# Kernel tuning notes

Measured on AMD Instinct MI355X. Metric: run time of the kernel, lower is better.

Reference implementation:

```python
import jax, jax.numpy as jnp
import numpy as np
from jax import lax

B, T, H = 2, 1024, 2048
NH, D = 8, 128          # heads, head_dim
P = NH * D              # projection size
K = 4                   # short conv kernel size
EPS = 1e-6
SCALE = D ** -0.5


def _causal_conv_silu(x, w):
    # x: (B,T,C); w: (C,K) depthwise causal conv followed by silu (ShortConvolution)
    C = w.shape[0]
    kern = jnp.transpose(w)[:, None, :]  # (K,1,C)
    y = lax.conv_general_dilated(x, kern, window_strides=(1,), padding=[(K - 1, 0)],
                                 dimension_numbers=('NWC', 'WIO', 'NWC'),
                                 feature_group_count=C)
    return jax.nn.silu(y)


def _l2norm(x):
    return x * jax.lax.rsqrt(jnp.sum(x * x, axis=-1, keepdims=True) + EPS)


def _forward(hidden_states, Wq, Wk, Wv, conv_q, conv_k, conv_v, A_log, dt_bias,
             Wfa, Wfb, Wb, Wga, Wgb, norm_weight, Wo):
    x = hidden_states                                # (B,T,H)
    q = _causal_conv_silu(x @ Wq.T, conv_q)          # (B,T,P)
    k = _causal_conv_silu(x @ Wk.T, conv_k)
    v = _causal_conv_silu(x @ Wv.T, conv_v)
    # fused_kda_gate: g = -exp(A_log) * softplus(f_b(f_a(x)) + dt_bias), per (h,d) channel
    gf = (x @ Wfa.T) @ Wfb.T                         # (B,T,P) low-rank gate proj
    gf = gf.reshape(B, T, NH, D) + dt_bias.reshape(NH, D)
    g = -jnp.exp(A_log)[None, None, :, None] * jax.nn.softplus(gf)  # (B,T,NH,D) log-decay <= 0
    beta = jax.nn.sigmoid(x @ Wb.T)                  # (B,T,NH)
    q = _l2norm(q.reshape(B, T, NH, D)) * SCALE      # use_qk_l2norm_in_kernel + 1/sqrt(d) scale
    k = _l2norm(k.reshape(B, T, NH, D))
    v = v.reshape(B, T, NH, D)

    # gated delta-rule recurrence (KDA): per-key-channel decay, beta-weighted delta update
    def step(S, inp):
        q_t, k_t, v_t, g_t, b_t = inp                # (B,NH,D), beta (B,NH)
        S = S * jnp.exp(g_t)[..., None]              # decay rows (key dim) of S[.,.,dk,dv]
        kv = jnp.einsum('bhk,bhkv->bhv', k_t, S)
        delta = (v_t - kv) * b_t[..., None]
        S = S + jnp.einsum('bhk,bhv->bhkv', k_t, delta)
        o_t = jnp.einsum('bhk,bhkv->bhv', q_t, S)
        return S, o_t

    tfirst = lambda a: jnp.moveaxis(a, 1, 0)         # time-major for scan
    S0 = jnp.zeros((B, NH, D, D), x.dtype)
    _, o = lax.scan(step, S0, (tfirst(q), tfirst(k), tfirst(v), tfirst(g), tfirst(beta)))
    o = jnp.moveaxis(o, 0, 1)                        # (B,T,NH,D)

    # FusedRMSNormGated(sigmoid): gate applied before RMS normalization (Mamba2 convention)
    gate = ((x @ Wga.T) @ Wgb.T).reshape(B, T, NH, D)
    og = o * jax.nn.sigmoid(gate)
    og = og * jax.lax.rsqrt(jnp.mean(og * og, axis=-1, keepdims=True) + EPS) * norm_weight
    return og.reshape(B * T, P) @ Wo.T               # (B*T, H)


def setup_inputs():
    ks = jax.random.split(jax.random.key(0), 16)
    s = 0.02
    f32 = jnp.float32
    return {
        'hidden_states': jax.random.normal(ks[0], (B, T, H), f32),
        'Wq': jax.random.normal(ks[1], (P, H), f32) * s,
        'Wk': jax.random.normal(ks[2], (P, H), f32) * s,
        'Wv': jax.random.normal(ks[3], (P, H), f32) * s,
        'conv_q': jax.random.normal(ks[4], (P, K), f32) * 0.3,
        'conv_k': jax.random.normal(ks[5], (P, K), f32) * 0.3,
        'conv_v': jax.random.normal(ks[6], (P, K), f32) * 0.3,
        'A_log': jnp.log(jax.random.uniform(ks[7], (NH,), f32, 1.0, 16.0)),
        'dt_bias': jax.random.normal(ks[8], (P,), f32) * 0.5,
        'Wfa': jax.random.normal(ks[9], (D, H), f32) * s,
        'Wfb': jax.random.normal(ks[10], (P, D), f32) * s,
        'Wb': jax.random.normal(ks[11], (NH, H), f32) * s,
        'Wga': jax.random.normal(ks[12], (D, H), f32) * s,
        'Wgb': jax.random.normal(ks[13], (P, D), f32) * s,
        'norm_weight': jnp.ones((D,), f32),
        'Wo': jax.random.normal(ks[14], (H, P), f32) * s,
    }


def reference(hidden_states, Wq, Wk, Wv, conv_q, conv_k, conv_v, A_log, dt_bias,
              Wfa, Wfb, Wb, Wga, Wgb, norm_weight, Wo):
    return _forward(hidden_states, Wq, Wk, Wv, conv_q, conv_k, conv_v, A_log, dt_bias,
                    Wfa, Wfb, Wb, Wga, Wgb, norm_weight, Wo)
```

## Files before the change

### kernel.cpp

```cpp
#include <hip/hip_runtime.h>
#include <hip/hip_bf16.h>
#include <cstddef>
#include <cstdint>

#define Bb 2
#define Tt 1024
#define Hh 2048
#define NHh 8
#define Dd 128
#define Pp (NHh * Dd)
#define Kk 4
#define EPSf 1e-6f
#define SCALEf 0.08838834764831845f
#define DVQ 16
#define CHUNK 8

typedef short bf16x8 __attribute__((ext_vector_type(8)));
typedef float f32x4 __attribute__((ext_vector_type(4)));

template <int CTRL>
__device__ __forceinline__ float dpp_add(float x) {
  int yi = __builtin_amdgcn_update_dpp(0, __builtin_bit_cast(int, x), CTRL, 0xF, 0xF, true);
  return x + __builtin_bit_cast(float, yi);
}
__device__ __forceinline__ float row16_sum(float x) {
  x = dpp_add<0xB1>(x);
  x = dpp_add<0x4E>(x);
  x = dpp_add<0x124>(x);
  x = dpp_add<0x128>(x);
  return x;
}

__device__ __forceinline__ void gload_lds16(const void* g, void* l) {
  __builtin_amdgcn_global_load_lds((const __attribute__((address_space(1))) void*)g,
                                   (__attribute__((address_space(3))) void*)l, 16, 0, 0);
}

__global__ __launch_bounds__(256) void cvt_bf16(const float* __restrict__ src,
                                                __hip_bfloat16* __restrict__ dst, int n) {
  const int i = (blockIdx.x * 256 + threadIdx.x) * 8;
  if (i >= n) return;
  const float4 a = *reinterpret_cast<const float4*>(src + i);
  const float4 b = *reinterpret_cast<const float4*>(src + i + 4);
  __hip_bfloat16 t[8];
  t[0] = __float2bfloat16(a.x); t[1] = __float2bfloat16(a.y);
  t[2] = __float2bfloat16(a.z); t[3] = __float2bfloat16(a.w);
  t[4] = __float2bfloat16(b.x); t[5] = __float2bfloat16(b.y);
  t[6] = __float2bfloat16(b.z); t[7] = __float2bfloat16(b.w);
  *reinterpret_cast<uint4*>(dst + i) = *reinterpret_cast<const uint4*>(t);
}

__global__ __launch_bounds__(256) void cvt_split(const float* __restrict__ src,
                                                 __hip_bfloat16* __restrict__ hi,
                                                 __hip_bfloat16* __restrict__ lo, int n) {
  const int i = (blockIdx.x * 256 + threadIdx.x) * 8;
  if (i >= n) return;
  __hip_bfloat16 th[8], tl[8];
#pragma unroll
  for (int j = 0; j < 2; j++) {
    const float4 a = *reinterpret_cast<const float4*>(src + i + j * 4);
    const float f[4] = {a.x, a.y, a.z, a.w};
#pragma unroll
    for (int e = 0; e < 4; e++) {
      const __hip_bfloat16 h = __float2bfloat16(f[e]);
      th[j * 4 + e] = h;
      tl[j * 4 + e] = __float2bfloat16(f[e] - __bfloat162float(h));
    }
  }
  *reinterpret_cast<uint4*>(hi + i) = *reinterpret_cast<const uint4*>(th);
  *reinterpret_cast<uint4*>(lo + i) = *reinterpret_cast<const uint4*>(tl);
}

__global__ __launch_bounds__(256) void transpose_f32(const float* __restrict__ src,
                                                     float* __restrict__ dst, int R, int C) {
  __shared__ float t[32][33];
  const int bx = blockIdx.x * 32, by = blockIdx.y * 32;
  const int tx = threadIdx.x & 31, ty = threadIdx.x >> 5;
#pragma unroll
  for (int i = ty; i < 32; i += 8) {
    const int r = by + i, c = bx + tx;
    if (r < R && c < C) t[i][tx] = src[(size_t)r * C + c];
  }
  __syncthreads();
#pragma unroll
  for (int i = ty; i < 32; i += 8) {
    const int c = bx + i, r = by + tx;
    if (c < C && r < R) dst[(size_t)c * R + r] = t[tx][i];
  }
}

__global__ __launch_bounds__(256) void gemm_bf16_lds(const __hip_bfloat16* __restrict__ A,
                                                     const __hip_bfloat16* __restrict__ B,
                                                     float* __restrict__ C,
                                                     __hip_bfloat16* __restrict__ Cbf,
                                                     int M, int N, int K, int outmode) {
  __shared__ __align__(16) __hip_bfloat16 As[128 * 64];
  __shared__ __align__(16) __hip_bfloat16 Bs[128 * 64];
  const int tid = threadIdx.x;
  const int wave = tid >> 6;
  const int lane = tid & 63;
  const int wm = (wave >> 1) * 64;
  const int wn = (wave & 1) * 64;
  const int bm = blockIdx.y * 128;
  const int bn = blockIdx.x * 128;
  const int l15 = lane & 15;
  const int l4 = lane >> 4;
  const int srow = lane >> 3;
  const int scol = (lane & 7) * 8;

  f32x4 acc[4][4];
#pragma unroll
  for (int i = 0; i < 4; i++)
#pragma unroll
    for (int j = 0; j < 4; j++) acc[i][j] = (f32x4){0.f, 0.f, 0.f, 0.f};

  for (int k0 = 0; k0 < K; k0 += 64) {
#pragma unroll
    for (int i = 0; i < 4; i++) {
      const int s = wave * 4 + i;
      const int row = s * 8 + srow;
      gload_lds16(A + (size_t)(bm + row) * K + k0 + scol, &As[s * 512]);
      gload_lds16(B + (size_t)(bn + row) * K + k0 + scol, &Bs[s * 512]);
    }
    __syncthreads();
    bf16x8 af[4][2], bfv[4][2];
#pragma unroll
    for (int kf = 0; kf < 2; kf++) {
      const int kc = kf * 32 + l4 * 8;
#pragma unroll
      for (int mf = 0; mf < 4; mf++)
        af[mf][kf] = *reinterpret_cast<const bf16x8*>(&As[(wm + mf * 16 + l15) * 64 + kc]);
#pragma unroll
      for (int nf = 0; nf < 4; nf++)
        bfv[nf][kf] = *reinterpret_cast<const bf16x8*>(&Bs[(wn + nf * 16 + l15) * 64 + kc]);
    }
#pragma unroll
    for (int kf = 0; kf < 2; kf++)
#pragma unroll
      for (int mf = 0; mf < 4; mf++)
#pragma unroll
        for (int nf = 0; nf < 4; nf++)
          acc[mf][nf] = __builtin_amdgcn_mfma_f32_16x16x32_bf16(af[mf][kf], bfv[nf][kf],
                                                                acc[mf][nf], 0, 0, 0);
    __syncthreads();
  }
#pragma unroll
  for (int mf = 0; mf < 4; mf++) {
#pragma unroll
    for (int nf = 0; nf < 4; nf++) {
      const int col = bn + wn + nf * 16 + l15;
#pragma unroll
      for (int r = 0; r < 4; r++) {
        const int row = bm + wm + mf * 16 + l4 * 4 + r;
        if (outmode == 0) C[(size_t)row * N + col] = acc[mf][nf][r];
        else Cbf[(size_t)row * N + col] = __float2bfloat16(acc[mf][nf][r]);
      }
    }
  }
}

#define LDT3 40
__global__ __launch_bounds__(256) void gemm_bf16_3t(const __hip_bfloat16* __restrict__ Ahi,
                                                    const __hip_bfloat16* __restrict__ Alo,
                                                    const __hip_bfloat16* __restrict__ Bhi,
                                                    const __hip_bfloat16* __restrict__ Blo,
                                                    float* __restrict__ C,
                                                    int M, int N, int K) {
  __shared__ __align__(16) __hip_bfloat16 Ahs[64][LDT3];
  __shared__ __align__(16) __hip_bfloat16 Als[64][LDT3];
  __shared__ __align__(16) __hip_bfloat16 Bhs[128][LDT3];
  __shared__ __align__(16) __hip_bfloat16 Bls[128][LDT3];
  const int tid = threadIdx.x;
  const int wave = tid >> 6;
  const int lane = tid & 63;
  const int wm = (wave >> 1) * 32;
  const int wn = (wave & 1) * 64;
  const int bm = blockIdx.y * 64;
  const int bn = blockIdx.x * 128;
  const int l15 = lane & 15;
  const int l4 = lane >> 4;
  const int arow = tid >> 2;
  const int acol = (tid & 3) * 8;

  f32x4 acc[2][4];
#pragma unroll
  for (int i = 0; i < 2; i++)
#pragma unroll
    for (int j = 0; j < 4; j++) acc[i][j] = (f32x4){0.f, 0.f, 0.f, 0.f};

  for (int k0 = 0; k0 < K; k0 += 32) {
    uint4 rah, ral, rbh0, rbh1, rbl0, rbl1;
    rah  = *reinterpret_cast<const uint4*>(Ahi + (size_t)(bm + arow) * K + k0 + acol);
    ral  = *reinterpret_cast<const uint4*>(Alo + (size_t)(bm + arow) * K + k0 + acol);
    rbh0 = *reinterpret_cast<const uint4*>(Bhi + (size_t)(bn + arow) * K + k0 + acol);
    rbh1 = *reinterpret_cast<const uint4*>(Bhi + (size_t)(bn + arow + 64) * K + k0 + acol);
    rbl0 = *reinterpret_cast<const uint4*>(Blo + (size_t)(bn + arow) * K + k0 + acol);
    rbl1 = *reinterpret_cast<const uint4*>(Blo + (size_t)(bn + arow + 64) * K + k0 + acol);
    __syncthreads();
    *reinterpret_cast<uint4*>(&Ahs[arow][acol]) = rah;
    *reinterpret_cast<uint4*>(&Als[arow][acol]) = ral;
    *reinterpret_cast<uint4*>(&Bhs[arow][acol]) = rbh0;
    *reinterpret_cast<uint4*>(&Bhs[arow + 64][acol]) = rbh1;
    *reinterpret_cast<uint4*>(&Bls[arow][acol]) = rbl0;
    *reinterpret_cast<uint4*>(&Bls[arow + 64][acol]) = rbl1;
    __syncthreads();
    const int kc = l4 * 8;
    bf16x8 ah[2], al[2], bhf[4], blf[4];
#pragma unroll
    for (int mf = 0; mf < 2; mf++) {
      ah[mf] = *reinterpret_cast<const bf16x8*>(&Ahs[wm + mf * 16 + l15][kc]);
      al[mf] = *reinterpret_cast<const bf16x8*>(&Als[wm + mf * 16 + l15][kc]);
    }
#pragma unroll
    for (int nf = 0; nf < 4; nf++) {
      bhf[nf] = *reinterpret_cast<const bf16x8*>(&Bhs[wn + nf * 16 + l15][kc]);
      blf[nf] = *reinterpret_cast<const bf16x8*>(&Bls[wn + nf * 16 + l15][kc]);
    }
#pragma unroll
    for (int mf = 0; mf < 2; mf++)
#pragma unroll
      for (int nf = 0; nf < 4; nf++) {
        acc[mf][nf] = __builtin_amdgcn_mfma_f32_16x16x32_bf16(ah[mf], bhf[nf], acc[mf][nf], 0, 0, 0);
        acc[mf][nf] = __builtin_amdgcn_mfma_f32_16x16x32_bf16(ah[mf], blf[nf], acc[mf][nf], 0, 0, 0);
        acc[mf][nf] = __builtin_amdgcn_mfma_f32_16x16x32_bf16(al[mf], bhf[nf], acc[mf][nf], 0, 0, 0);
      }
  }
#pragma unroll
  for (int mf = 0; mf < 2; mf++)
#pragma unroll
    for (int nf = 0; nf < 4; nf++) {
      const int col = bn + wn + nf * 16 + l15;
#pragma unroll
      for (int r = 0; r < 4; r++) {
        const int row = bm + wm + mf * 16 + l4 * 4 + r;
        C[(size_t)row * N + col] = acc[mf][nf][r];
      }
    }
}

__global__ __launch_bounds__(256) void gemm_nt(const float* __restrict__ A,
                                               const float* __restrict__ Bm,
                                               float* __restrict__ C,
                                               int M, int N, int Kd) {
  __shared__ float As[16][64];
  __shared__ float Bs[16][64];
  const int bm = blockIdx.y * 64;
  const int bn = blockIdx.x * 64;
  const int tid = threadIdx.x;
  const int tx = tid & 15;
  const int ty = tid >> 4;
  const int lr = tid >> 2;
  const int lc = (tid & 3) << 2;
  float acc[4][4];
#pragma unroll
  for (int i = 0; i < 4; i++)
#pragma unroll
    for (int j = 0; j < 4; j++) acc[i][j] = 0.f;
  for (int k0 = 0; k0 < Kd; k0 += 16) {
    float4 a4 = make_float4(0.f, 0.f, 0.f, 0.f);
    float4 b4 = make_float4(0.f, 0.f, 0.f, 0.f);
    const int ar = bm + lr;
    if (ar < M) a4 = *reinterpret_cast<const float4*>(A + (size_t)ar * Kd + k0 + lc);
    const int br = bn + lr;
    if (br < N) b4 = *reinterpret_cast<const float4*>(Bm + (size_t)br * Kd + k0 + lc);
    As[lc + 0][lr] = a4.x; As[lc + 1][lr] = a4.y; As[lc + 2][lr] = a4.z; As[lc + 3][lr] = a4.w;
    Bs[lc + 0][lr] = b4.x; Bs[lc + 1][lr] = b4.y; Bs[lc + 2][lr] = b4.z; Bs[lc + 3][lr] = b4.w;
    __syncthreads();
#pragma unroll
    for (int kk = 0; kk < 16; kk++) {
      float4 av = *reinterpret_cast<const float4*>(&As[kk][ty << 2]);
      float4 bv = *reinterpret_cast<const float4*>(&Bs[kk][tx << 2]);
      float a[4] = {av.x, av.y, av.z, av.w};
      float b[4] = {bv.x, bv.y, bv.z, bv.w};
#pragma unroll
      for (int i = 0; i < 4; i++)
#pragma unroll
        for (int j = 0; j < 4; j++) acc[i][j] += a[i] * b[j];
    }
    __syncthreads();
  }
#pragma unroll
  for (int i = 0; i < 4; i++) {
    const int row = bm + (ty << 2) + i;
    if (row >= M) continue;
#pragma unroll
    for (int j = 0; j < 4; j++) {
      const int col = bn + (tx << 2) + j;
      if (col < N) C[(size_t)row * N + col] = acc[i][j];
    }
  }
}

__global__ __launch_bounds__(256) void beta_kernel(const float* __restrict__ x,
                                                   const float* __restrict__ Wb,
                                                   float* __restrict__ beta) {
  __shared__ float xs[Hh];
  const int m = blockIdx.x;
  const int tid = threadIdx.x;
  for (int i = tid; i < Hh; i += 256) xs[i] = x[(size_t)m * Hh + i];
  __syncthreads();
  const int h = tid >> 5;
  const int lane = tid & 31;
  float acc = 0.f;
  for (int i = lane; i < Hh; i += 32) acc += xs[i] * Wb[(size_t)h * Hh + i];
#pragma unroll
  for (int o = 16; o > 0; o >>= 1) acc += __shfl_down(acc, o, 32);
  if (lane == 0) beta[(size_t)m * NHh + h] = 1.f / (1.f + expf(-acc));
}

__global__ __launch_bounds__(256) void g_kernel(float* __restrict__ gbuf,
                                                const float* __restrict__ dtb,
                                                const float* __restrict__ A_log) {
  const size_t i = (size_t)blockIdx.x * 256 + threadIdx.x;
  const int c = (int)(i % Pp);
  const int h = c / Dd;
  const float xv = gbuf[i] + dtb[c];
  const float sp = (xv > 20.f) ? xv : log1pf(expf(xv));
  gbuf[i] = expf(-expf(A_log[h]) * sp);
}

__global__ __launch_bounds__(128) void conv_silu_norm(const float* __restrict__ xin,
                                                      const float* __restrict__ w,
                                                      float* __restrict__ out,
                                                      int mode, int instride, int coff) {
  const int idx = blockIdx.x;
  const int h = idx % NHh;
  const int bt = idx / NHh;
  const int t = bt % Tt;
  const int d = threadIdx.x;
  const int c = h * Dd + d;
  float acc = 0.f;
#pragma unroll
  for (int j = 0; j < Kk; j++) {
    const int tt = t - (Kk - 1) + j;
    float xv = 0.f;
    if (tt >= 0) xv = xin[(size_t)(bt - (Kk - 1) + j) * instride + coff + c];
    acc += w[c * Kk + j] * xv;
  }
  float y = acc / (1.f + expf(-acc));
  float r = y;
  if (mode > 0) {
    float ss = y * y;
#pragma unroll
    for (int o = 32; o > 0; o >>= 1) ss += __shfl_down(ss, o);
    __shared__ float red[2];
    if ((d & 63) == 0) red[d >> 6] = ss;
    __syncthreads();
    const float tot = red[0] + red[1];
    const float inv = rsqrtf(tot + EPSf);
    r = y * inv * (mode == 2 ? SCALEf : 1.f);
  }
  out[(size_t)bt * Pp + c] = r;
}

__global__ __launch_bounds__(128) void scan_kernel(const float* __restrict__ q,
                                                   const float* __restrict__ k,
                                                   const float* __restrict__ v,
                                                   const float* __restrict__ eg,
                                                   const float* __restrict__ beta,
                                                   float* __restrict__ o) {
  const int blk = blockIdx.x;
  const int bh = blk & 15;
  const int dvq = blk >> 4;
  const int b = bh >> 3, h = bh & 7;
  const int tid = threadIdx.x;
  const int qr = tid & 15;
  const int dvl = tid >> 4;
  const int dv = dvq * 8 + dvl;

  __shared__ __align__(16) float qs[CHUNK][16][12];
  __shared__ __align__(16) float ks[CHUNK][16][12];
  __shared__ __align__(16) float legs[CHUNK][16][12];
  __shared__ float vs[CHUNK][8];
  __shared__ float betas[CHUNK];

  float s[8];
#pragma unroll
  for (int i = 0; i < 8; i++) s[i] = 0.f;

  const size_t base = (size_t)(b * Tt) * Pp + h * Dd;
  const int le = tid;

  float rq[CHUNK], rk[CHUNK], re[CHUNK], rv[CHUNK], rb;
  auto load_chunk = [&](int t0) {
    const size_t coff = base + (size_t)t0 * Pp;
#pragma unroll
    for (int j = 0; j < CHUNK; j++) {
      rq[j] = q[coff + (size_t)j * Pp + le];
      rk[j] = k[coff + (size_t)j * Pp + le];
      re[j] = eg[coff + (size_t)j * Pp + le];
    }
    if (tid < 8) {
#pragma unroll
      for (int j = 0; j < CHUNK; j++) rv[j] = v[coff + (size_t)j * Pp + dvq * 8 + tid];
    } else if (tid < 8 + CHUNK) {
      rb = beta[(size_t)(b * Tt + t0 + tid - 8) * NHh + h];
    }
  };

  load_chunk(0);
  size_t off = base;
  for (int c = 0; c < Tt / CHUNK; c++) {
    __syncthreads();
#pragma unroll
    for (int j = 0; j < CHUNK; j++) {
      qs[j][le >> 3][le & 7] = rq[j];
      ks[j][le >> 3][le & 7] = rk[j];
      legs[j][le >> 3][le & 7] = re[j];
    }
    if (tid < 8) {
#pragma unroll
      for (int j = 0; j < CHUNK; j++) vs[j][tid] = rv[j];
    } else if (tid < 8 + CHUNK) {
      betas[tid - 8] = rb;
    }
    __syncthreads();
    if (c + 1 < Tt / CHUNK) load_chunk((c + 1) * CHUNK);

    float vv[CHUNK], bb[CHUNK], opart[CHUNK];
#pragma unroll
    for (int j = 0; j < CHUNK; j++) { vv[j] = vs[j][dvl]; bb[j] = betas[j]; }

#pragma unroll
    for (int j = 0; j < CHUNK; j++) {
      const float4 k0 = *reinterpret_cast<const float4*>(&ks[j][qr][0]);
      const float4 k1 = *reinterpret_cast<const float4*>(&ks[j][qr][4]);
      const float4 e0 = *reinterpret_cast<const float4*>(&legs[j][qr][0]);
      const float4 e1 = *reinterpret_cast<const float4*>(&legs[j][qr][4]);
      s[0] *= e0.x; s[1] *= e0.y; s[2] *= e0.z; s[3] *= e0.w;
      s[4] *= e1.x; s[5] *= e1.y; s[6] *= e1.z; s[7] *= e1.w;
      float kva = k0.x * s[0] + k1.x * s[4];
      float kvb = k0.y * s[1] + k1.y * s[5];
      float kvc = k0.z * s[2] + k1.z * s[6];
      float kvd = k0.w * s[3] + k1.w * s[7];
      const float kvp = row16_sum((kva + kvb) + (kvc + kvd));
      const float delta = (vv[j] - kvp) * bb[j];
      const float4 q0 = *reinterpret_cast<const float4*>(&qs[j][qr][0]);
      const float4 q1 = *reinterpret_cast<const float4*>(&qs[j][qr][4]);
      s[0] += k0.x * delta; float oa = q0.x * s[0];
      s[1] += k0.y * delta; float ob = q0.y * s[1];
      s[2] += k0.z * delta; float oc = q0.z * s[2];
      s[3] += k0.w * delta; float od = q0.w * s[3];
      s[4] += k1.x * delta; oa += q1.x * s[4];
      s[5] += k1.y * delta; ob += q1.y * s[5];
      s[6] += k1.z * delta; oc += q1.z * s[6];
      s[7] += k1.w * delta; od += q1.w * s[7];
      opart[j] = (oa + ob) + (oc + od);
    }
#pragma unroll
    for (int j = 0; j < CHUNK; j++) opart[j] = row16_sum(opart[j]);
    if (qr == 0) {
#pragma unroll
      for (int j = 0; j < CHUNK; j++) o[off + (size_t)j * Pp + dv] = opart[j];
    }
    off += (size_t)CHUNK * Pp;
  }
}

__global__ __launch_bounds__(128) void gated_norm(float* __restrict__ o,
                                                  const float* __restrict__ gate,
                                                  int gstride,
                                                  const float* __restrict__ nw,
                                                  __hip_bfloat16* __restrict__ ogbf) {
  const int idx = blockIdx.x;
  const int h = idx % NHh;
  const int bt = idx / NHh;
  const int d = threadIdx.x;
  const size_t off = (size_t)bt * Pp + h * Dd;
  const float ov = o[off + d];
  const float gt = gate[(size_t)bt * gstride + h * Dd + d];
  const float val = ov / (1.f + expf(-gt));
  float ss = val * val;
#pragma unroll
  for (int sh = 32; sh > 0; sh >>= 1) ss += __shfl_down(ss, sh);
  __shared__ float red[2];
  if ((d & 63) == 0) red[d >> 6] = ss;
  __syncthreads();
  const float mean = (red[0] + red[1]) * (1.f / Dd);
  const float res = val * rsqrtf(mean + EPSf) * nw[d];
  if (ogbf != nullptr) ogbf[off + d] = __float2bfloat16(res);
  else o[off + d] = res;
}

extern "C" void kernel_launch(void* const* d_in, const int* in_sizes, int n_in,
                              void* d_out, int out_size, void* d_ws, size_t ws_size,
                              hipStream_t stream) {
  const float* x     = (const float*)d_in[0];
  const float* Wq    = (const float*)d_in[1];
  const float* Wk    = (const float*)d_in[2];
  const float* Wv    = (const float*)d_in[3];
  const float* cq    = (const float*)d_in[4];
  const float* ck    = (const float*)d_in[5];
  const float* cv    = (const float*)d_in[6];
  const float* A_log = (const float*)d_in[7];
  const float* dtb   = (const float*)d_in[8];
  const float* Wfa   = (const float*)d_in[9];
  const float* Wfb   = (const float*)d_in[10];
  const float* Wb    = (const float*)d_in[11];
  const float* Wga   = (const float*)d_in[12];
  const float* Wgb   = (const float*)d_in[13];
  const float* nw    = (const float*)d_in[14];
  const float* Wo    = (const float*)d_in[15];
  float* outp = (float*)d_out;

  const int M = Bb * Tt;
  const size_t MP = (size_t)M * Pp;
  float* ws = (float*)d_ws;
  float* qkvpre = ws;
  float* qb   = qkvpre + 4 * MP;
  float* kb   = qb + MP;
  float* vb   = kb + MP;
  float* gbuf = vb + MP;
  float* obuf = gbuf + MP;
  float* betab = obuf + MP;
  float* WfaT = betab + (size_t)M * NHh;
  float* WgaT = WfaT + (size_t)Hh * Dd;
  float* f32end = WgaT + (size_t)Hh * Dd;
  float* Wcombf = obuf;

  __hip_bfloat16* xhi    = (__hip_bfloat16*)f32end;
  __hip_bfloat16* xlo    = xhi + (size_t)M * Hh;
  __hip_bfloat16* Wqkvbf = xlo + (size_t)M * Hh;
  __hip_bfloat16* Wobf   = Wqkvbf + (size_t)4 * Pp * Hh;
  __hip_bfloat16* WfaThi = Wobf + (size_t)Hh * Pp;
  __hip_bfloat16* WfaTlo = WfaThi + (size_t)Hh * Dd;
  __hip_bfloat16* Wfbhi  = WfaTlo + (size_t)Hh * Dd;
  __hip_bfloat16* Wfblo  = Wfbhi + (size_t)Pp * Dd;
  __hip_bfloat16* WgaTbf = Wfblo + (size_t)Pp * Dd;
  __hip_bfloat16* Wgbbf  = WgaTbf + (size_t)Hh * Dd;
  __hip_bfloat16* Wcombhi = Wgbbf + (size_t)Pp * Dd;
  __hip_bfloat16* Wcomblo = Wcombhi + (size_t)Pp * Hh;
  __hip_bfloat16* end = Wcomblo + (size_t)Pp * Hh;
  __hip_bfloat16* ogbf = xlo;
  const bool use_mfma = ws_size >= (size_t)((char*)end - (char*)d_ws);

  const dim3 blk(256);
  if (use_mfma) {
    cvt_split<<<(int)((size_t)M * Hh / 2048), blk, 0, stream>>>(x, xhi, xlo, M * Hh);
    cvt_bf16<<<(int)((size_t)Pp * Hh / 2048), blk, 0, stream>>>(Wq, Wqkvbf, Pp * Hh);
    cvt_bf16<<<(int)((size_t)Pp * Hh / 2048), blk, 0, stream>>>(Wk, Wqkvbf + (size_t)Pp * Hh, Pp * Hh);
    cvt_bf16<<<(int)((size_t)Pp * Hh / 2048), blk, 0, stream>>>(Wv, Wqkvbf + (size_t)2 * Pp * Hh, Pp * Hh);
    cvt_bf16<<<(int)((size_t)Hh * Pp / 2048), blk, 0, stream>>>(Wo, Wobf, Hh * Pp);
    transpose_f32<<<dim3(Hh / 32, Dd / 32), blk, 0, stream>>>(Wfa, WfaT, Dd, Hh);
    transpose_f32<<<dim3(Hh / 32, Dd / 32), blk, 0, stream>>>(Wga, WgaT, Dd, Hh);
    cvt_split<<<(int)((size_t)Hh * Dd / 2048), blk, 0, stream>>>(WfaT, WfaThi, WfaTlo, Hh * Dd);
    cvt_split<<<(int)((size_t)Pp * Dd / 2048), blk, 0, stream>>>(Wfb, Wfbhi, Wfblo, Pp * Dd);
    cvt_bf16<<<(int)((size_t)Hh * Dd / 2048), blk, 0, stream>>>(WgaT, WgaTbf, Hh * Dd);
    cvt_bf16<<<(int)((size_t)Pp * Dd / 2048), blk, 0, stream>>>(Wgb, Wgbbf, Pp * Dd);
    gemm_bf16_3t<<<dim3(Hh / 128, Pp / 64), blk, 0, stream>>>(Wfbhi, Wfblo, WfaThi, WfaTlo,
                                                              Wcombf, Pp, Hh, Dd);
    gemm_bf16_lds<<<dim3(Hh / 128, Pp / 128), blk, 0, stream>>>(Wgbbf, WgaTbf, nullptr,
                                                                Wqkvbf + (size_t)3 * Pp * Hh,
                                                                Pp, Hh, Dd, 1);
    cvt_split<<<(int)((size_t)Pp * Hh / 2048), blk, 0, stream>>>(Wcombf, Wcombhi, Wcomblo, Pp * Hh);
    gemm_bf16_lds<<<dim3(4 * Pp / 128, M / 128), blk, 0, stream>>>(xhi, Wqkvbf, qkvpre, nullptr,
                                                                   M, 4 * Pp, Hh, 0);
    gemm_bf16_3t<<<dim3(Pp / 128, M / 64), blk, 0, stream>>>(xhi, xlo, Wcombhi, Wcomblo,
                                                             gbuf, M, Pp, Hh);
    beta_kernel<<<M, 256, 0, stream>>>(x, Wb, betab);
    g_kernel<<<(int)(MP / 256), 256, 0, stream>>>(gbuf, dtb, A_log);
    conv_silu_norm<<<M * NHh, 128, 0, stream>>>(qkvpre, cq, qb, 2, 4 * Pp, 0);
    conv_silu_norm<<<M * NHh, 128, 0, stream>>>(qkvpre, ck, kb, 1, 4 * Pp, Pp);
    conv_silu_norm<<<M * NHh, 128, 0, stream>>>(qkvpre, cv, vb, 0, 4 * Pp, 2 * Pp);
    scan_kernel<<<Bb * NHh * DVQ, 128, 0, stream>>>(qb, kb, vb, gbuf, betab, obuf);
    gated_norm<<<M * NHh, 128, 0, stream>>>(obuf, qkvpre + (size_t)3 * Pp, 4 * Pp, nw, ogbf);
    gemm_bf16_lds<<<dim3(Hh / 128, M / 128), blk, 0, stream>>>(ogbf, Wobf, outp, nullptr, M, Hh, Pp, 0);
  } else {
    float* qpre = qkvpre;
    float* kpre = qkvpre + MP;
    float* vpre = qkvpre + 2 * MP;
    float* gate = qkvpre + 3 * MP;
    float* gfa = WfaT;
    float* gga = WgaT;
    gemm_nt<<<dim3(Pp / 64, M / 64), blk, 0, stream>>>(x, Wq, qpre, M, Pp, Hh);
    gemm_nt<<<dim3(Pp / 64, M / 64), blk, 0, stream>>>(x, Wk, kpre, M, Pp, Hh);
    gemm_nt<<<dim3(Pp / 64, M / 64), blk, 0, stream>>>(x, Wv, vpre, M, Pp, Hh);
    gemm_nt<<<dim3(Dd / 64, M / 64), blk, 0, stream>>>(x, Wfa, gfa, M, Dd, Hh);
    gemm_nt<<<dim3(Dd / 64, M / 64), blk, 0, stream>>>(x, Wga, gga, M, Dd, Hh);
    gemm_nt<<<dim3(Pp / 64, M / 64), blk, 0, stream>>>(gfa, Wfb, gbuf, M, Pp, Dd);
    gemm_nt<<<dim3(Pp / 64, M / 64), blk, 0, stream>>>(gga, Wgb, gate, M, Pp, Dd);
    beta_kernel<<<M, 256, 0, stream>>>(x, Wb, betab);
    g_kernel<<<(int)(MP / 256), 256, 0, stream>>>(gbuf, dtb, A_log);
    conv_silu_norm<<<M * NHh, 128, 0, stream>>>(qpre, cq, qb, 2, Pp, 0);
    conv_silu_norm<<<M * NHh, 128, 0, stream>>>(kpre, ck, kb, 1, Pp, 0);
    conv_silu_norm<<<M * NHh, 128, 0, stream>>>(vpre, cv, vb, 0, Pp, 0);
    scan_kernel<<<Bb * NHh * DVQ, 128, 0, stream>>>(qb, kb, vb, gbuf, betab, obuf);
    gated_norm<<<M * NHh, 128, 0, stream>>>(obuf, gate, Pp, nw, nullptr);
    gemm_nt<<<dim3(Hh / 64, M / 64), blk, 0, stream>>>(obuf, Wo, outp, M, Hh, Pp);
  }
}
```

Baseline: 486.1 us.

## Double-buffer scan LDS, use direct-to-LDS loads in 3-term GEMM, batch weight casts

```diff
diff --git a/kernel.cpp b/kernel.cpp
--- a/kernel.cpp
+++ b/kernel.cpp
@@ -47,6 +47,30 @@
   t[2] = __float2bfloat16(a.z); t[3] = __float2bfloat16(a.w);
   t[4] = __float2bfloat16(b.x); t[5] = __float2bfloat16(b.y);
   t[6] = __float2bfloat16(b.z); t[7] = __float2bfloat16(b.w);
+  *reinterpret_cast<uint4*>(dst + i) = *reinterpret_cast<const uint4*>(t);
+}
+
+__global__ __launch_bounds__(256) void cvt_bf16_x4(const float* __restrict__ s0,
+                                                   const float* __restrict__ s1,
+                                                   const float* __restrict__ s2,
+                                                   const float* __restrict__ s3,
+                                                   __hip_bfloat16* __restrict__ d0,
+                                                   __hip_bfloat16* __restrict__ d1,
+                                                   __hip_bfloat16* __restrict__ d2,
+                                                   __hip_bfloat16* __restrict__ d3,
+                                                   int nper) {
+  const int bpa = nper / 2048;
+  const int a = blockIdx.x / bpa;
+  const int i = (blockIdx.x % bpa) * 2048 + threadIdx.x * 8;
+  const float* src = (a == 0) ? s0 : (a == 1) ? s1 : (a == 2) ? s2 : s3;
+  __hip_bfloat16* dst = (a == 0) ? d0 : (a == 1) ? d1 : (a == 2) ? d2 : d3;
+  const float4 x = *reinterpret_cast<const float4*>(src + i);
+  const float4 y = *reinterpret_cast<const float4*>(src + i + 4);
+  __hip_bfloat16 t[8];
+  t[0] = __float2bfloat16(x.x); t[1] = __float2bfloat16(x.y);
+  t[2] = __float2bfloat16(x.z); t[3] = __float2bfloat16(x.w);
+  t[4] = __float2bfloat16(y.x); t[5] = __float2bfloat16(y.y);
+  t[6] = __float2bfloat16(y.z); t[7] = __float2bfloat16(y.w);
   *reinterpret_cast<uint4*>(dst + i) = *reinterpret_cast<const uint4*>(t);
 }
 
@@ -159,17 +183,16 @@
   }
 }
 
-#define LDT3 40
-__global__ __launch_bounds__(256) void gemm_bf16_3t(const __hip_bfloat16* __restrict__ Ahi,
-                                                    const __hip_bfloat16* __restrict__ Alo,
-                                                    const __hip_bfloat16* __restrict__ Bhi,
-                                                    const __hip_bfloat16* __restrict__ Blo,
-                                                    float* __restrict__ C,
-                                                    int M, int N, int K) {
-  __shared__ __align__(16) __hip_bfloat16 Ahs[64][LDT3];
-  __shared__ __align__(16) __hip_bfloat16 Als[64][LDT3];
-  __shared__ __align__(16) __hip_bfloat16 Bhs[128][LDT3];
-  __shared__ __align__(16) __hip_bfloat16 Bls[128][LDT3];
+__global__ __launch_bounds__(256) void gemm_bf16_3t_lds(const __hip_bfloat16* __restrict__ Ahi,
+                                                        const __hip_bfloat16* __restrict__ Alo,
+                                                        const __hip_bfloat16* __restrict__ Bhi,
+                                                        const __hip_bfloat16* __restrict__ Blo,
+                                                        float* __restrict__ C,
+                                                        int M, int N, int K) {
+  __shared__ __align__(16) __hip_bfloat16 Ahs[64 * 64];
+  __shared__ __align__(16) __hip_bfloat16 Als[64 * 64];
+  __shared__ __align__(16) __hip_bfloat16 Bhs[128 * 64];
+  __shared__ __align__(16) __hip_bfloat16 Bls[128 * 64];
   const int tid = threadIdx.x;
   const int wave = tid >> 6;
   const int lane = tid & 63;
@@ -179,8 +202,8 @@
   const int bn = blockIdx.x * 128;
   const int l15 = lane & 15;
   const int l4 = lane >> 4;
-  const int arow = tid >> 2;
-  const int acol = (tid & 3) * 8;
+  const int srow = lane >> 3;
+  const int scol = (lane & 7) * 8;
 
   f32x4 acc[2][4];
 #pragma unroll
@@ -188,42 +211,49 @@
 #pragma unroll
     for (int j = 0; j < 4; j++) acc[i][j] = (f32x4){0.f, 0.f, 0.f, 0.f};
 
-  for (int k0 = 0; k0 < K; k0 += 32) {
-    uint4 rah, ral, rbh0, rbh1, rbl0, rbl1;
-    rah  = *reinterpret_cast<const uint4*>(Ahi + (size_t)(bm + arow) * K + k0 + acol);
-    ral  = *reinterpret_cast<const uint4*>(Alo + (size_t)(bm + arow) * K + k0 + acol);
-    rbh0 = *reinterpret_cast<const uint4*>(Bhi + (size_t)(bn + arow) * K + k0 + acol);
-    rbh1 = *reinterpret_cast<const uint4*>(Bhi + (size_t)(bn + arow + 64) * K + k0 + acol);
-    rbl0 = *reinterpret_cast<const uint4*>(Blo + (size_t)(bn + arow) * K + k0 + acol);
-    rbl1 = *reinterpret_cast<const uint4*>(Blo + (size_t)(bn + arow + 64) * K + k0 + acol);
-    __syncthreads();
-    *reinterpret_cast<uint4*>(&Ahs[arow][acol]) = rah;
-    *reinterpret_cast<uint4*>(&Als[arow][acol]) = ral;
-    *reinterpret_cast<uint4*>(&Bhs[arow][acol]) = rbh0;
-    *reinterpret_cast<uint4*>(&Bhs[arow + 64][acol]) = rbh1;
-    *reinterpret_cast<uint4*>(&Bls[arow][acol]) = rbl0;
-    *reinterpret_cast<uint4*>(&Bls[arow + 64][acol]) = rbl1;
-    __syncthreads();
-    const int kc = l4 * 8;
-    bf16x8 ah[2], al[2], bhf[4], blf[4];
-#pragma unroll
-    for (int mf = 0; mf < 2; mf++) {
-      ah[mf] = *reinterpret_cast<const bf16x8*>(&Ahs[wm + mf * 16 + l15][kc]);
-      al[mf] = *reinterpret_cast<const bf16x8*>(&Als[wm + mf * 16 + l15][kc]);
-    }
-#pragma unroll
-    for (int nf = 0; nf < 4; nf++) {
-      bhf[nf] = *reinterpret_cast<const bf16x8*>(&Bhs[wn + nf * 16 + l15][kc]);
-      blf[nf] = *reinterpret_cast<const bf16x8*>(&Bls[wn + nf * 16 + l15][kc]);
-    }
-#pragma unroll
-    for (int mf = 0; mf < 2; mf++)
+  for (int k0 = 0; k0 < K; k0 += 64) {
+#pragma unroll
+    for (int i = 0; i < 12; i++) {
+      const int sid = wave * 12 + i;
+      if (sid < 8) {
+        const int row = sid * 8 + srow;
+        gload_lds16(Ahi + (size_t)(bm + row) * K + k0 + scol, &Ahs[sid * 512]);
+      } else if (sid < 16) {
+        const int row = (sid - 8) * 8 + srow;
+        gload_lds16(Alo + (size_t)(bm + row) * K + k0 + scol, &Als[(sid - 8) * 512]);
+      } else if (sid < 32) {
+        const int row = (sid - 16) * 8 + srow;
+        gload_lds16(Bhi + (size_t)(bn + row) * K + k0 + scol, &Bhs[(sid - 16) * 512]);
+      } else {
+        const int row = (sid - 32) * 8 + srow;
+        gload_lds16(Blo + (size_t)(bn + row) * K + k0 + scol, &Bls[(sid - 32) * 512]);
+      }
+    }
+    __syncthreads();
+#pragma unroll
+    for (int kf = 0; kf < 2; kf++) {
+      const int kc = kf * 32 + l4 * 8;
+      bf16x8 ah[2], al[2], bh[4], bl[4];
+#pragma unroll
+      for (int mf = 0; mf < 2; mf++) {
+        ah[mf] = *reinterpret_cast<const bf16x8*>(&Ahs[(wm + mf * 16 + l15) * 64 + kc]);
+        al[mf] = *reinterpret_cast<const bf16x8*>(&Als[(wm + mf * 16 + l15) * 64 + kc]);
+      }
 #pragma unroll
       for (int nf = 0; nf < 4; nf++) {
-        acc[mf][nf] = __builtin_amdgcn_mfma_f32_16x16x32_bf16(ah[mf], bhf[nf], acc[mf][nf], 0, 0, 0);
-        acc[mf][nf] = __builtin_amdgcn_mfma_f32_16x16x32_bf16(ah[mf], blf[nf], acc[mf][nf], 0, 0, 0);
-        acc[mf][nf] = __builtin_amdgcn_mfma_f32_16x16x32_bf16(al[mf], bhf[nf], acc[mf][nf], 0, 0, 0);
+        bh[nf] = *reinterpret_cast<const bf16x8*>(&Bhs[(wn + nf * 16 + l15) * 64 + kc]);
+        bl[nf] = *reinterpret_cast<const bf16x8*>(&Bls[(wn + nf * 16 + l15) * 64 + kc]);
       }
+#pragma unroll
+      for (int mf = 0; mf < 2; mf++)
+#pragma unroll
+        for (int nf = 0; nf < 4; nf++) {
+          acc[mf][nf] = __builtin_amdgcn_mfma_f32_16x16x32_bf16(ah[mf], bh[nf], acc[mf][nf], 0, 0, 0);
+          acc[mf][nf] = __builtin_amdgcn_mfma_f32_16x16x32_bf16(ah[mf], bl[nf], acc[mf][nf], 0, 0, 0);
+          acc[mf][nf] = __builtin_amdgcn_mfma_f32_16x16x32_bf16(al[mf], bh[nf], acc[mf][nf], 0, 0, 0);
+        }
+    }
+    __syncthreads();
   }
 #pragma unroll
   for (int mf = 0; mf < 2; mf++)
@@ -368,11 +398,11 @@
   const int dvl = tid >> 4;
   const int dv = dvq * 8 + dvl;
 
-  __shared__ __align__(16) float qs[CHUNK][16][12];
-  __shared__ __align__(16) float ks[CHUNK][16][12];
-  __shared__ __align__(16) float legs[CHUNK][16][12];
-  __shared__ float vs[CHUNK][8];
-  __shared__ float betas[CHUNK];
+  __shared__ __align__(16) float qs[2][CHUNK][16][12];
+  __shared__ __align__(16) float ks[2][CHUNK][16][12];
+  __shared__ __align__(16) float legs[2][CHUNK][16][12];
+  __shared__ float vs[2][CHUNK][8];
+  __shared__ float betas[2][CHUNK];
 
   float s[8];
 #pragma unroll
@@ -381,7 +411,7 @@
   const size_t base = (size_t)(b * Tt) * Pp + h * Dd;
   const int le = tid;
 
-  float rq[CHUNK], rk[CHUNK], re[CHUNK], rv[CHUNK], rb;
+  float rq[CHUNK], rk[CHUNK], re[CHUNK], rv[CHUNK], rb = 0.f;
   auto load_chunk = [&](int t0) {
     const size_t coff = base + (size_t)t0 * Pp;
 #pragma unroll
@@ -397,55 +427,75 @@
       rb = beta[(size_t)(b * Tt + t0 + tid - 8) * NHh + h];
     }
   };
+  auto write_lds = [&](int bufw) {
+#pragma unroll
+    for (int j = 0; j < CHUNK; j++) {
+      qs[bufw][j][le >> 3][le & 7] = rq[j];
+      ks[bufw][j][le >> 3][le & 7] = rk[j];
+      legs[bufw][j][le >> 3][le & 7] = re[j];
+    }
+    if (tid < 8) {
+#pragma unroll
+      for (int j = 0; j < CHUNK; j++) vs[bufw][j][tid] = rv[j];
+    } else if (tid < 8 + CHUNK) {
+      betas[bufw][tid - 8] = rb;
+    }
+  };
 
   load_chunk(0);
+  write_lds(0);
+  __syncthreads();
+  const int NC = Tt / CHUNK;
   size_t off = base;
-  for (int c = 0; c < Tt / CHUNK; c++) {
-    __syncthreads();
+  for (int c = 0; c < NC; c++) {
+    if (c + 1 < NC) load_chunk((c + 1) * CHUNK);
+    const int buf = c & 1;
+    float vv[CHUNK], bb[CHUNK], opart[CHUNK];
+#pragma unroll
+    for (int j = 0; j < CHUNK; j++) { vv[j] = vs[buf][j][dvl]; bb[j] = betas[buf][j]; }
+
+    float4 ck0 = *reinterpret_cast<const float4*>(&ks[buf][0][qr][0]);
+    float4 ck1 = *reinterpret_cast<const float4*>(&ks[buf][0][qr][4]);
+    float4 ce0 = *reinterpret_cast<const float4*>(&legs[buf][0][qr][0]);
+    float4 ce1 = *reinterpret_cast<const float4*>(&legs[buf][0][qr][4]);
+    float4 cq0 = *reinterpret_cast<const float4*>(&qs[buf][0][qr][0]);
+    float4 cq1 = *reinterpret_cast<const float4*>(&qs[buf][0][qr][4]);
+    float kt0 = ck0.x * ce0.x, kt1 = ck0.y * ce0.y, kt2 = ck0.z * ce0.z, kt3 = ck0.w * ce0.w;
+    float kt4 = ck1.x * ce1.x, kt5 = ck1.y * ce1.y, kt6 = ck1.z * ce1.z, kt7 = ck1.w * ce1.w;
+
 #pragma unroll
     for (int j = 0; j < CHUNK; j++) {
-      qs[j][le >> 3][le & 7] = rq[j];
-      ks[j][le >> 3][le & 7] = rk[j];
-      legs[j][le >> 3][le & 7] = re[j];
-    }
-    if (tid < 8) {
-#pragma unroll
-      for (int j = 0; j < CHUNK; j++) vs[j][tid] = rv[j];
-    } else if (tid < 8 + CHUNK) {
-      betas[tid - 8] = rb;
-    }
-    __syncthreads();
-    if (c + 1 < Tt / CHUNK) load_chunk((c + 1) * CHUNK);
-
-    float vv[CHUNK], bb[CHUNK], opart[CHUNK];
-#pragma unroll
-    for (int j = 0; j < CHUNK; j++) { vv[j] = vs[j][dvl]; bb[j] = betas[j]; }
-
-#pragma unroll
-    for (int j = 0; j < CHUNK; j++) {
-      const float4 k0 = *reinterpret_cast<const float4*>(&ks[j][qr][0]);
-      const float4 k1 = *reinterpret_cast<const float4*>(&ks[j][qr][4]);
-      const float4 e0 = *reinterpret_cast<const float4*>(&legs[j][qr][0]);
-      const float4 e1 = *reinterpret_cast<const float4*>(&legs[j][qr][4]);
-      s[0] *= e0.x; s[1] *= e0.y; s[2] *= e0.z; s[3] *= e0.w;
-      s[4] *= e1.x; s[5] *= e1.y; s[6] *= e1.z; s[7] *= e1.w;
-      float kva = k0.x * s[0] + k1.x * s[4];
-      float kvb = k0.y * s[1] + k1.y * s[5];
-      float kvc = k0.z * s[2] + k1.z * s[6];
-      float kvd = k0.w * s[3] + k1.w * s[7];
+      float4 nk0, nk1, ne0, ne1, nq0, nq1;
+      if (j + 1 < CHUNK) {
+        nk0 = *reinterpret_cast<const float4*>(&ks[buf][j + 1][qr][0]);
+        nk1 = *reinterpret_cast<const float4*>(&ks[buf][j + 1][qr][4]);
+        ne0 = *reinterpret_cast<const float4*>(&legs[buf][j + 1][qr][0]);
+        ne1 = *reinterpret_cast<const float4*>(&legs[buf][j + 1][qr][4]);
+        nq0 = *reinterpret_cast<const float4*>(&qs[buf][j + 1][qr][0]);
+        nq1 = *reinterpret_cast<const float4*>(&qs[buf][j + 1][qr][4]);
+      }
+      const float es0 = ce0.x * s[0], es1 = ce0.y * s[1], es2 = ce0.z * s[2], es3 = ce0.w * s[3];
+      const float es4 = ce1.x * s[4], es5 = ce1.y * s[5], es6 = ce1.z * s[6], es7 = ce1.w * s[7];
+      float kva = kt0 * s[0] + kt4 * s[4];
+      float kvb = kt1 * s[1] + kt5 * s[5];
+      float kvc = kt2 * s[2] + kt6 * s[6];
+      float kvd = kt3 * s[3] + kt7 * s[7];
       const float kvp = row16_sum((kva + kvb) + (kvc + kvd));
       const float delta = (vv[j] - kvp) * bb[j];
-      const float4 q0 = *reinterpret_cast<const float4*>(&qs[j][qr][0]);
-      const float4 q1 = *reinterpret_cast<const float4*>(&qs[j][qr][4]);
-      s[0] += k0.x * delta; float oa = q0.x * s[0];
-      s[1] += k0.y * delta; float ob = q0.y * s[1];
-      s[2] += k0.z * delta; float oc = q0.z * s[2];
-      s[3] += k0.w * delta; float od = q0.w * s[3];
-      s[4] += k1.x * delta; oa += q1.x * s[4];
-      s[5] += k1.y * delta; ob += q1.y * s[5];
-      s[6] += k1.z * delta; oc += q1.z * s[6];
-      s[7] += k1.w * delta; od += q1.w * s[7];
+      s[0] = fmaf(ck0.x, delta, es0); float oa = cq0.x * s[0];
+      s[1] = fmaf(ck0.y, delta, es1); float ob = cq0.y * s[1];
+      s[2] = fmaf(ck0.z, delta, es2); float oc = cq0.z * s[2];
+      s[3] = fmaf(ck0.w, delta, es3); float od = cq0.w * s[3];
+      s[4] = fmaf(ck1.x, delta, es4); oa += cq1.x * s[4];
+      s[5] = fmaf(ck1.y, delta, es5); ob += cq1.y * s[5];
+      s[6] = fmaf(ck1.z, delta, es6); oc += cq1.z * s[6];
+      s[7] = fmaf(ck1.w, delta, es7); od += cq1.w * s[7];
       opart[j] = (oa + ob) + (oc + od);
+      if (j + 1 < CHUNK) {
+        ck0 = nk0; ck1 = nk1; ce0 = ne0; ce1 = ne1; cq0 = nq0; cq1 = nq1;
+        kt0 = ck0.x * ce0.x; kt1 = ck0.y * ce0.y; kt2 = ck0.z * ce0.z; kt3 = ck0.w * ce0.w;
+        kt4 = ck1.x * ce1.x; kt5 = ck1.y * ce1.y; kt6 = ck1.z * ce1.z; kt7 = ck1.w * ce1.w;
+      }
     }
 #pragma unroll
     for (int j = 0; j < CHUNK; j++) opart[j] = row16_sum(opart[j]);
@@ -453,6 +503,8 @@
 #pragma unroll
       for (int j = 0; j < CHUNK; j++) o[off + (size_t)j * Pp + dv] = opart[j];
     }
+    if (c + 1 < NC) write_lds(buf ^ 1);
+    __syncthreads();
     off += (size_t)CHUNK * Pp;
   }
 }
@@ -537,26 +589,25 @@
   const dim3 blk(256);
   if (use_mfma) {
     cvt_split<<<(int)((size_t)M * Hh / 2048), blk, 0, stream>>>(x, xhi, xlo, M * Hh);
-    cvt_bf16<<<(int)((size_t)Pp * Hh / 2048), blk, 0, stream>>>(Wq, Wqkvbf, Pp * Hh);
-    cvt_bf16<<<(int)((size_t)Pp * Hh / 2048), blk, 0, stream>>>(Wk, Wqkvbf + (size_t)Pp * Hh, Pp * Hh);
-    cvt_bf16<<<(int)((size_t)Pp * Hh / 2048), blk, 0, stream>>>(Wv, Wqkvbf + (size_t)2 * Pp * Hh, Pp * Hh);
-    cvt_bf16<<<(int)((size_t)Hh * Pp / 2048), blk, 0, stream>>>(Wo, Wobf, Hh * Pp);
+    cvt_bf16_x4<<<4 * (int)((size_t)Pp * Hh / 2048), blk, 0, stream>>>(
+        Wq, Wk, Wv, Wo, Wqkvbf, Wqkvbf + (size_t)Pp * Hh, Wqkvbf + (size_t)2 * Pp * Hh,
+        Wobf, Pp * Hh);
     transpose_f32<<<dim3(Hh / 32, Dd / 32), blk, 0, stream>>>(Wfa, WfaT, Dd, Hh);
     transpose_f32<<<dim3(Hh / 32, Dd / 32), blk, 0, stream>>>(Wga, WgaT, Dd, Hh);
     cvt_split<<<(int)((size_t)Hh * Dd / 2048), blk, 0, stream>>>(WfaT, WfaThi, WfaTlo, Hh * Dd);
     cvt_split<<<(int)((size_t)Pp * Dd / 2048), blk, 0, stream>>>(Wfb, Wfbhi, Wfblo, Pp * Dd);
     cvt_bf16<<<(int)((size_t)Hh * Dd / 2048), blk, 0, stream>>>(WgaT, WgaTbf, Hh * Dd);
     cvt_bf16<<<(int)((size_t)Pp * Dd / 2048), blk, 0, stream>>>(Wgb, Wgbbf, Pp * Dd);
-    gemm_bf16_3t<<<dim3(Hh / 128, Pp / 64), blk, 0, stream>>>(Wfbhi, Wfblo, WfaThi, WfaTlo,
-                                                              Wcombf, Pp, Hh, Dd);
+    gemm_bf16_3t_lds<<<dim3(Hh / 128, Pp / 64), blk, 0, stream>>>(Wfbhi, Wfblo, WfaThi, WfaTlo,
+                                                                  Wcombf, Pp, Hh, Dd);
     gemm_bf16_lds<<<dim3(Hh / 128, Pp / 128), blk, 0, stream>>>(Wgbbf, WgaTbf, nullptr,
                                                                 Wqkvbf + (size_t)3 * Pp * Hh,
                                                                 Pp, Hh, Dd, 1);
     cvt_split<<<(int)((size_t)Pp * Hh / 2048), blk, 0, stream>>>(Wcombf, Wcombhi, Wcomblo, Pp * Hh);
     gemm_bf16_lds<<<dim3(4 * Pp / 128, M / 128), blk, 0, stream>>>(xhi, Wqkvbf, qkvpre, nullptr,
                                                                    M, 4 * Pp, Hh, 0);
-    gemm_bf16_3t<<<dim3(Pp / 128, M / 64), blk, 0, stream>>>(xhi, xlo, Wcombhi, Wcomblo,
-                                                             gbuf, M, Pp, Hh);
+    gemm_bf16_3t_lds<<<dim3(Pp / 128, M / 64), blk, 0, stream>>>(xhi, xlo, Wcombhi, Wcomblo,
+                                                                 gbuf, M, Pp, Hh);
     beta_kernel<<<M, 256, 0, stream>>>(x, Wb, betab);
     g_kernel<<<(int)(MP / 256), 256, 0, stream>>>(gbuf, dtb, A_log);
     conv_silu_norm<<<M * NHh, 128, 0, stream>>>(qkvpre, cq, qb, 2, 4 * Pp, 0);
```

New measurement: 470.3 us. 1.03x faster.
